# Performance work log

Measured on AMD Instinct MI355X. Metric: run time of the kernel, lower is better.

The kernel has to match this reference:

```python
import jax, jax.numpy as jnp
import numpy as np

N = 100_000      # nodes
E = 1_600_000    # edges
NG = 512         # graphs in batch
EPS = 1e-5


def _prop(x, src, dst, n, add_self_loops):
    """GCN-normalized sparse propagation: agg_i = sum_{j->i} d_j^-1/2 d_i^-1/2 x_j."""
    ones = jnp.ones(src.shape[0], x.dtype)
    deg = jax.ops.segment_sum(ones, dst, num_segments=n)
    if add_self_loops:
        deg = deg + 1.0
    dinv = jnp.where(deg > 0, jax.lax.rsqrt(jnp.maximum(deg, 1e-12)), 0.0)
    w = dinv[src] * dinv[dst]                       # [E]
    agg = jax.ops.segment_sum(x[src] * w[:, None], dst, num_segments=n)
    if add_self_loops:
        agg = agg + x * (dinv * dinv)[:, None]
    return agg


def setup_inputs() -> dict:
    key = jax.random.key(0)
    ks = jax.random.split(key, 24)
    w = lambda k, s: jax.random.normal(k, s, jnp.float32) * 0.05
    dim = 100
    return {
        "x": jax.random.normal(ks[0], (N, 128), jnp.float32),
        "src": jax.random.randint(ks[1], (E,), 0, N),
        "dst": jax.random.randint(ks[2], (E,), 0, N),
        "batch": jnp.sort(jax.random.randint(ks[3], (N,), 0, NG)),
        # SGConv 1 & 2 (propagate then Linear)
        "W1": w(ks[4], (128, dim)), "b1": jnp.zeros((dim,), jnp.float32),
        "W2": w(ks[5], (dim, dim)), "b2": jnp.zeros((dim,), jnp.float32),
        # BatchNorm1d affine params
        "gamma": jnp.ones((dim,), jnp.float32), "beta": jnp.zeros((dim,), jnp.float32),
        # ARMAConv (num_stacks=1, num_layers=1)
        "Wa_init": w(ks[6], (dim, dim)), "Wa_root": w(ks[7], (dim, dim)),
        "ba": jnp.zeros((dim,), jnp.float32),
        # MLP head
        "Wf1": w(ks[8], (dim, 2 * dim)), "bf1": jnp.zeros((2 * dim,), jnp.float32),
        "Wf2": w(ks[9], (2 * dim, 3 * dim)), "bf2": jnp.zeros((3 * dim,), jnp.float32),
        "Wf3": w(ks[10], (3 * dim, 2 * dim)), "bf3": jnp.zeros((2 * dim,), jnp.float32),
        "Wf4": w(ks[11], (2 * dim, 1)), "bf4": jnp.zeros((1,), jnp.float32),
    }


def reference(x, src, dst, batch, W1, b1, W2, b2, gamma, beta,
              Wa_init, Wa_root, ba, Wf1, bf1, Wf2, bf2, Wf3, bf3, Wf4, bf4):
    n = x.shape[0]
    # SGConv (K=1): propagate with self-loop gcn_norm, then linear; ReLU
    h = jax.nn.relu(_prop(x, src, dst, n, True) @ W1 + b1)
    h = jax.nn.relu(_prop(h, src, dst, n, True) @ W2 + b2)
    # BatchNorm1d (training mode: batch statistics, biased var)
    mu = jnp.mean(h, axis=0)
    var = jnp.mean((h - mu) ** 2, axis=0)
    h = (h - mu) * jax.lax.rsqrt(var + EPS) * gamma + beta
    # ARMAConv (1 stack, 1 layer): ReLU(A_hat (h W_init) + h W_root + b), no self-loops
    a = jax.nn.relu(_prop(h @ Wa_init, src, dst, n, False) + h @ Wa_root + ba)
    # global_add_pool over graph ids
    g = jax.ops.segment_sum(a, batch, num_segments=NG)   # [NG, dim]
    # MLP head
    g = jax.nn.relu(g @ Wf1 + bf1)
    g = jax.nn.relu(g @ Wf2 + bf2)
    g = jax.nn.relu(g @ Wf3 + bf3)
    return g @ Wf4 + bf4
```

## Files before the change

kernel.cpp:

```cpp
#include <hip/hip_runtime.h>
#include <hip/hip_fp16.h>

#define NNODES 100000
#define NEDGES 1600000
#define NGRAPH 512
#define DIM    100
#define DP     128
#define EPSBN  1e-5f
#define NBUK   ((NNODES + 255) >> 8)
#define BINCH  8192

typedef _Float16 half8 __attribute__((ext_vector_type(8)));
typedef float floatx4 __attribute__((ext_vector_type(4)));

__global__ __launch_bounds__(256) void bin_count_kernel(const int* __restrict__ dst,
                                                        int* __restrict__ btotal, int e) {
    __shared__ int lc[NBUK];
    int tid = threadIdx.x;
    int base = blockIdx.x * BINCH;
    int m = e - base; if (m > BINCH) m = BINCH;
    for (int b = tid; b < NBUK; b += 256) lc[b] = 0;
    __syncthreads();
    for (int j = tid; j < m; j += 256)
        atomicAdd(&lc[dst[base + j] >> 8], 1);
    __syncthreads();
    for (int b = tid; b < NBUK; b += 256)
        if (lc[b]) atomicAdd(&btotal[b], lc[b]);
}

__global__ void bucket_scan_kernel(const int* __restrict__ btotal, int* __restrict__ bbase,
                                   int* __restrict__ bcursor, int e) {
    __shared__ int s[512];
    int tid = threadIdx.x;
    int v = (tid < NBUK) ? btotal[tid] : 0;
    s[tid] = v; __syncthreads();
    for (int o = 1; o < 512; o <<= 1) {
        int t = (tid >= o) ? s[tid - o] : 0;
        __syncthreads();
        s[tid] += t;
        __syncthreads();
    }
    if (tid < NBUK) {
        int base = s[tid] - v;
        bbase[tid] = base;
        bcursor[tid] = base;
    }
    if (tid == 0) bbase[NBUK] = e;
}

__global__ __launch_bounds__(256) void bin_kernel(
        const int* __restrict__ src, const int* __restrict__ dst,
        int* __restrict__ bcursor, int2* __restrict__ gpairs, int e) {
    __shared__ int2 lpairs[BINCH];
    __shared__ int lcount[NBUK], lstart[NBUK], lcur[NBUK], gbase[NBUK];
    int tid = threadIdx.x;
    int base = blockIdx.x * BINCH;
    int m = e - base; if (m > BINCH) m = BINCH;

    for (int b = tid; b < NBUK; b += 256) lcount[b] = 0;
    __syncthreads();

    for (int j = tid; j < m; j += 256)
        atomicAdd(&lcount[dst[base + j] >> 8], 1);
    __syncthreads();

    if (tid == 0) {
        int acc = 0;
        for (int b = 0; b < NBUK; b++) {
            lstart[b] = acc;
            lcur[b] = acc;
            acc += lcount[b];
        }
    }
    __syncthreads();

    for (int b = tid; b < NBUK; b += 256)
        gbase[b] = atomicAdd(&bcursor[b], lcount[b]);
    for (int j = tid; j < m; j += 256) {
        int s = src[base + j], d = dst[base + j];
        int p = atomicAdd(&lcur[d >> 8], 1);
        lpairs[p] = make_int2(s, d);
    }
    __syncthreads();

    for (int j = tid; j < m; j += 256) {
        int2 pr = lpairs[j];
        int b = pr.y >> 8;
        gpairs[gbase[b] + (j - lstart[b])] = pr;
    }
}

__global__ __launch_bounds__(256) void bucket_build_kernel(
        const int2* __restrict__ gpairs, const int* __restrict__ bbase,
        int* __restrict__ off, int* __restrict__ ssorted,
        float* __restrict__ dsl, float* __restrict__ dnsl, int n, int e) {
    __shared__ int cnt[256];
    __shared__ int sc[256];
    int b = blockIdx.x, tid = threadIdx.x;
    int node0 = b << 8;
    int e0 = bbase[b], e1 = bbase[b + 1];

    cnt[tid] = 0;
    __syncthreads();
    for (int j = e0 + tid; j < e1; j += 256)
        atomicAdd(&cnt[gpairs[j].y & 255], 1);
    __syncthreads();

    int c = cnt[tid];
    sc[tid] = c; __syncthreads();
    for (int o = 1; o < 256; o <<= 1) {
        int t = (tid >= o) ? sc[tid - o] : 0;
        __syncthreads();
        sc[tid] += t;
        __syncthreads();
    }
    int excl = sc[tid] - c;

    int node = node0 + tid;
    if (node < n) {
        off[node] = e0 + excl;
        float cf = (float)c;
        dsl[node] = rsqrtf(cf + 1.0f);
        dnsl[node] = (c > 0) ? rsqrtf(cf) : 0.0f;
    }
    if (b == NBUK - 1 && tid == 0) off[n] = e;

    __syncthreads();
    cnt[tid] = e0 + excl;
    __syncthreads();
    for (int j = e0 + tid; j < e1; j += 256) {
        int2 pr = gpairs[j];
        int p = atomicAdd(&cnt[pr.y & 255], 1);
        ssorted[p] = pr.x;
    }
}

__global__ void prescale_kernel(const float* __restrict__ x, const float* __restrict__ d,
                                __half* __restrict__ yh, int n) {
    long i = (long)blockIdx.x * blockDim.x + threadIdx.x;
    if (i >= (long)n * 32) return;
    int row = (int)(i >> 5);
    float s = d[row];
    float4 v = ((const float4*)x)[i];
    __half2 p01 = __floats2half2_rn(v.x * s, v.y * s);
    __half2 p23 = __floats2half2_rn(v.z * s, v.w * s);
    uint2 u;
    u.x = *(unsigned int*)&p01;
    u.y = *(unsigned int*)&p23;
    ((uint2*)yh)[i] = u;
}

__global__ void packW_kernel(const float* __restrict__ W, _Float16* __restrict__ WtF,
                             int K, int Kout) {
    int idx = blockIdx.x * 256 + threadIdx.x;
    if (idx >= DP * DP) return;
    int j = idx & 7;
    int l = (idx >> 3) & 63;
    int c = idx >> 9;
    int t = c >> 2, k0 = c & 3;
    int nn = t * 16 + (l & 15);
    int k = k0 * 32 + (l >> 4) * 8 + j;
    float v = (k < K && nn < Kout) ? W[k * Kout + nn] : 0.f;
    WtF[idx] = (_Float16)v;
}

__global__ __launch_bounds__(256) void prop_kernel(
        const __half* __restrict__ pre, const int* __restrict__ ssorted,
        const int* __restrict__ off, const float* __restrict__ dinv,
        __half* __restrict__ outH, int n, int selfloop) {
    int wave = (blockIdx.x * blockDim.x + threadIdx.x) >> 6;
    int lane = threadIdx.x & 63;
    if (wave >= n) return;
    int e0 = off[wave], e1 = off[wave + 1];
    int deg = e1 - e0;
    int g = lane >> 4;
    int q = lane & 15;

    float acc[8];
#pragma unroll
    for (int i = 0; i < 8; i++) acc[i] = 0.f;

    auto addu = [&](uint4 u) {
        float2 f;
        f = __half22float2(*(__half2*)&u.x); acc[0] += f.x; acc[1] += f.y;
        f = __half22float2(*(__half2*)&u.y); acc[2] += f.x; acc[3] += f.y;
        f = __half22float2(*(__half2*)&u.z); acc[4] += f.x; acc[5] += f.y;
        f = __half22float2(*(__half2*)&u.w); acc[6] += f.x; acc[7] += f.y;
    };
    auto rowptr = [&](int s) -> const uint4* {
        return (const uint4*)&pre[(long)s * DP + q * 8];
    };

    for (int base = 0; base < deg; base += 64) {
        int m = deg - base; if (m > 64) m = 64;
        int sidx = (lane < m) ? ssorted[e0 + base + lane] : 0;
        int j = 0;
        for (; j + 16 <= m; j += 16) {
            int s0 = __shfl(sidx, j + g);
            int s1 = __shfl(sidx, j + 4 + g);
            int s2 = __shfl(sidx, j + 8 + g);
            int s3 = __shfl(sidx, j + 12 + g);
            uint4 u0 = *rowptr(s0);
            uint4 u1 = *rowptr(s1);
            uint4 u2 = *rowptr(s2);
            uint4 u3 = *rowptr(s3);
            addu(u0); addu(u1); addu(u2); addu(u3);
        }
        for (; j + 4 <= m; j += 4) {
            int s = __shfl(sidx, j + g);
            addu(*rowptr(s));
        }
        if (j < m) {
            int r = m - j;
            int s = __shfl(sidx, (g < r) ? j + g : j);
            if (g < r) addu(*rowptr(s));
        }
    }

#pragma unroll
    for (int i = 0; i < 8; i++) {
        acc[i] += __shfl_xor(acc[i], 16);
        acc[i] += __shfl_xor(acc[i], 32);
    }

    if (g == 0) {
        float dn = dinv[wave];
        if (selfloop) addu(*rowptr(wave));
        __half2 p0 = __floats2half2_rn(dn * acc[0], dn * acc[1]);
        __half2 p1 = __floats2half2_rn(dn * acc[2], dn * acc[3]);
        __half2 p2 = __floats2half2_rn(dn * acc[4], dn * acc[5]);
        __half2 p3 = __floats2half2_rn(dn * acc[6], dn * acc[7]);
        uint4 u;
        u.x = *(unsigned int*)&p0;
        u.y = *(unsigned int*)&p1;
        u.z = *(unsigned int*)&p2;
        u.w = *(unsigned int*)&p3;
        *(uint4*)&outH[(long)wave * DP + q * 8] = u;
    }
}

__global__ __launch_bounds__(256) void prop_arma_kernel(
        const __half* __restrict__ pre, const int* __restrict__ ssorted,
        const int* __restrict__ off, const float* __restrict__ dinv,
        const __half* __restrict__ R, __half* __restrict__ outH, int n) {
    int wave = (blockIdx.x * blockDim.x + threadIdx.x) >> 6;
    int lane = threadIdx.x & 63;
    if (wave >= n) return;
    int e0 = off[wave], e1 = off[wave + 1];
    int deg = e1 - e0;
    int g = lane >> 4;
    int q = lane & 15;

    float acc[8];
#pragma unroll
    for (int i = 0; i < 8; i++) acc[i] = 0.f;

    auto addu = [&](uint4 u) {
        float2 f;
        f = __half22float2(*(__half2*)&u.x); acc[0] += f.x; acc[1] += f.y;
        f = __half22float2(*(__half2*)&u.y); acc[2] += f.x; acc[3] += f.y;
        f = __half22float2(*(__half2*)&u.z); acc[4] += f.x; acc[5] += f.y;
        f = __half22float2(*(__half2*)&u.w); acc[6] += f.x; acc[7] += f.y;
    };
    auto rowptr = [&](int s) -> const uint4* {
        return (const uint4*)&pre[(long)s * DP + q * 8];
    };

    for (int base = 0; base < deg; base += 64) {
        int m = deg - base; if (m > 64) m = 64;
        int sidx = (lane < m) ? ssorted[e0 + base + lane] : 0;
        int j = 0;
        for (; j + 16 <= m; j += 16) {
            int s0 = __shfl(sidx, j + g);
            int s1 = __shfl(sidx, j + 4 + g);
            int s2 = __shfl(sidx, j + 8 + g);
            int s3 = __shfl(sidx, j + 12 + g);
            uint4 u0 = *rowptr(s0);
            uint4 u1 = *rowptr(s1);
            uint4 u2 = *rowptr(s2);
            uint4 u3 = *rowptr(s3);
            addu(u0); addu(u1); addu(u2); addu(u3);
        }
        for (; j + 4 <= m; j += 4) {
            int s = __shfl(sidx, j + g);
            addu(*rowptr(s));
        }
        if (j < m) {
            int r = m - j;
            int s = __shfl(sidx, (g < r) ? j + g : j);
            if (g < r) addu(*rowptr(s));
        }
    }

#pragma unroll
    for (int i = 0; i < 8; i++) {
        acc[i] += __shfl_xor(acc[i], 16);
        acc[i] += __shfl_xor(acc[i], 32);
    }

    if (g == 0) {
        float dn = dinv[wave];
        uint4 r4 = *(const uint4*)&R[(long)wave * DP + q * 8];
        float rr[8];
        float2 f;
        f = __half22float2(*(__half2*)&r4.x); rr[0] = f.x; rr[1] = f.y;
        f = __half22float2(*(__half2*)&r4.y); rr[2] = f.x; rr[3] = f.y;
        f = __half22float2(*(__half2*)&r4.z); rr[4] = f.x; rr[5] = f.y;
        f = __half22float2(*(__half2*)&r4.w); rr[6] = f.x; rr[7] = f.y;
        float o[8];
#pragma unroll
        for (int i = 0; i < 8; i++) o[i] = fmaxf(dn * acc[i] + rr[i], 0.f);
        __half2 p0 = __floats2half2_rn(o[0], o[1]);
        __half2 p1 = __floats2half2_rn(o[2], o[3]);
        __half2 p2 = __floats2half2_rn(o[4], o[5]);
        __half2 p3 = __floats2half2_rn(o[6], o[7]);
        uint4 u;
        u.x = *(unsigned int*)&p0;
        u.y = *(unsigned int*)&p1;
        u.z = *(unsigned int*)&p2;
        u.w = *(unsigned int*)&p3;
        *(uint4*)&outH[(long)wave * DP + q * 8] = u;
    }
}

__global__ __launch_bounds__(256, 2) void matmul_mfma_kernel(
        const __half* __restrict__ A, const _Float16* __restrict__ WtF,
        const float* __restrict__ bias, const float* __restrict__ rowscale,
        __half* __restrict__ Ch, float* __restrict__ bnsum, float* __restrict__ bnsq,
        int M, int Kout, int relu) {
    __shared__ float Ct[64 * 132];
    int tid = threadIdx.x;
    int wave = tid >> 6;
    int lane = tid & 63;
    int m16 = lane & 15;
    int quad = lane >> 4;
    long row0blk = (long)blockIdx.x * 64;
    long row0 = row0blk + wave * 16;

    const half8* Bp = (const half8*)WtF;
    half8 bf[32];
#pragma unroll
    for (int c = 0; c < 32; c++) bf[c] = Bp[c * 64 + lane];

    half8 af[4];
    {
        long ar = row0 + m16; if (ar >= M) ar = M - 1;
        const _Float16* Ap = (const _Float16*)&A[ar * DP + quad * 8];
#pragma unroll
        for (int k0 = 0; k0 < 4; k0++)
            af[k0] = *(const half8*)(Ap + k0 * 32);
    }

    floatx4 acc[8];
#pragma unroll
    for (int t = 0; t < 8; t++) acc[t] = (floatx4){0.f, 0.f, 0.f, 0.f};

#pragma unroll
    for (int c = 0; c < 32; c++)
        acc[c >> 2] = __builtin_amdgcn_mfma_f32_16x16x32_f16(af[c & 3], bf[c], acc[c >> 2], 0, 0, 0);

    int lrow0 = wave * 16 + quad * 4;
#pragma unroll
    for (int t = 0; t < 8; t++)
#pragma unroll
        for (int r = 0; r < 4; r++)
            Ct[(lrow0 + r) * 132 + t * 16 + m16] = acc[t][r];
    __syncthreads();

    float s4[4] = {0.f, 0.f, 0.f, 0.f};
    float q4[4] = {0.f, 0.f, 0.f, 0.f};
    for (int idx = tid; idx < 64 * 32; idx += 256) {
        int lr = idx >> 5, c4 = idx & 31;
        long grow = row0blk + lr;
        if (grow >= M) continue;
        int col = c4 * 4;
        float4 v = *(const float4*)&Ct[lr * 132 + col];
        if (bias && col < Kout) {
            float4 bb = *(const float4*)&bias[col];
            v.x += bb.x; v.y += bb.y; v.z += bb.z; v.w += bb.w;
        }
        if (relu) {
            v.x = fmaxf(v.x, 0.f); v.y = fmaxf(v.y, 0.f);
            v.z = fmaxf(v.z, 0.f); v.w = fmaxf(v.w, 0.f);
        }
        if (rowscale) {
            float rs = rowscale[grow];
            v.x *= rs; v.y *= rs; v.z *= rs; v.w *= rs;
        }
        if (bnsum) {
            s4[0] += v.x; s4[1] += v.y; s4[2] += v.z; s4[3] += v.w;
            q4[0] += v.x * v.x; q4[1] += v.y * v.y; q4[2] += v.z * v.z; q4[3] += v.w * v.w;
        }
        __half2 p01 = __floats2half2_rn(v.x, v.y);
        __half2 p23 = __floats2half2_rn(v.z, v.w);
        uint2 u;
        u.x = *(unsigned int*)&p01;
        u.y = *(unsigned int*)&p23;
        *(uint2*)&Ch[grow * DP + col] = u;
    }

    if (bnsum) {
        __syncthreads();
        float* scr = Ct;
        int g = tid >> 5, c4 = tid & 31;
#pragma unroll
        for (int i = 0; i < 4; i++) {
            scr[g * 128 + c4 * 4 + i] = s4[i];
            scr[1024 + g * 128 + c4 * 4 + i] = q4[i];
        }
        __syncthreads();
        if (tid < 128) {
            float ss = 0.f, qq = 0.f;
#pragma unroll
            for (int gg = 0; gg < 8; gg++) {
                ss += scr[gg * 128 + tid];
                qq += scr[1024 + gg * 128 + tid];
            }
            atomicAdd(&bnsum[tid], ss);
            atomicAdd(&bnsq[tid], qq);
        }
    }
}

__global__ __launch_bounds__(256, 2) void matmul_dual_kernel(
        const __half* __restrict__ A, const _Float16* __restrict__ WtF3,
        const _Float16* __restrict__ WtF4, const float* __restrict__ ba,
        const float* __restrict__ rowscale,
        __half* __restrict__ Ch1, __half* __restrict__ ChR, int M, int Kout) {
    __shared__ float Ct[64 * 132];
    int tid = threadIdx.x;
    int wave = tid >> 6;
    int lane = tid & 63;
    int m16 = lane & 15;
    int quad = lane >> 4;
    long row0blk = (long)blockIdx.x * 64;
    long row0 = row0blk + wave * 16;

    half8 af[4];
    {
        long ar = row0 + m16; if (ar >= M) ar = M - 1;
        const _Float16* Ap = (const _Float16*)&A[ar * DP + quad * 8];
#pragma unroll
        for (int k0 = 0; k0 < 4; k0++)
            af[k0] = *(const half8*)(Ap + k0 * 32);
    }

    const half8* Bp3 = (const half8*)WtF3;
    const half8* Bp4 = (const half8*)WtF4;
    floatx4 acc3[8], acc4[8];
#pragma unroll
    for (int t = 0; t < 8; t++) {
        acc3[t] = (floatx4){0.f, 0.f, 0.f, 0.f};
        acc4[t] = (floatx4){0.f, 0.f, 0.f, 0.f};
    }

#pragma unroll
    for (int t = 0; t < 8; t++) {
        half8 b3[4], b4[4];
#pragma unroll
        for (int k0 = 0; k0 < 4; k0++) {
            b3[k0] = Bp3[(t * 4 + k0) * 64 + lane];
            b4[k0] = Bp4[(t * 4 + k0) * 64 + lane];
        }
#pragma unroll
        for (int k0 = 0; k0 < 4; k0++) {
            acc3[t] = __builtin_amdgcn_mfma_f32_16x16x32_f16(af[k0], b3[k0], acc3[t], 0, 0, 0);
            acc4[t] = __builtin_amdgcn_mfma_f32_16x16x32_f16(af[k0], b4[k0], acc4[t], 0, 0, 0);
        }
    }

    int lrow0 = wave * 16 + quad * 4;

#pragma unroll
    for (int t = 0; t < 8; t++)
#pragma unroll
        for (int r = 0; r < 4; r++)
            Ct[(lrow0 + r) * 132 + t * 16 + m16] = acc3[t][r];
    __syncthreads();
    for (int idx = tid; idx < 64 * 32; idx += 256) {
        int lr = idx >> 5, c4 = idx & 31;
        long grow = row0blk + lr;
        if (grow >= M) continue;
        int col = c4 * 4;
        float4 v = *(const float4*)&Ct[lr * 132 + col];
        float rs = rowscale[grow];
        v.x *= rs; v.y *= rs; v.z *= rs; v.w *= rs;
        __half2 p01 = __floats2half2_rn(v.x, v.y);
        __half2 p23 = __floats2half2_rn(v.z, v.w);
        uint2 u;
        u.x = *(unsigned int*)&p01;
        u.y = *(unsigned int*)&p23;
        *(uint2*)&Ch1[grow * DP + col] = u;
    }
    __syncthreads();

#pragma unroll
    for (int t = 0; t < 8; t++)
#pragma unroll
        for (int r = 0; r < 4; r++)
            Ct[(lrow0 + r) * 132 + t * 16 + m16] = acc4[t][r];
    __syncthreads();
    for (int idx = tid; idx < 64 * 32; idx += 256) {
        int lr = idx >> 5, c4 = idx & 31;
        long grow = row0blk + lr;
        if (grow >= M) continue;
        int col = c4 * 4;
        float4 v = *(const float4*)&Ct[lr * 132 + col];
        if (col < Kout) {
            float4 bb = *(const float4*)&ba[col];
            v.x += bb.x; v.y += bb.y; v.z += bb.z; v.w += bb.w;
        }
        __half2 p01 = __floats2half2_rn(v.x, v.y);
        __half2 p23 = __floats2half2_rn(v.z, v.w);
        uint2 u;
        u.x = *(unsigned int*)&p01;
        u.y = *(unsigned int*)&p23;
        *(uint2*)&ChR[grow * DP + col] = u;
    }
}

__global__ void bn_prep_kernel(const float* __restrict__ sum, const float* __restrict__ sq,
                               const float* __restrict__ gamma, const float* __restrict__ beta,
                               float* __restrict__ scale, float* __restrict__ shift, int n) {
    int c = threadIdx.x;
    float sc = 0.f, sh = 0.f;
    if (c < DIM) {
        float inv_n = 1.0f / (float)n;
        float mu = sum[c] * inv_n;
        float var = sq[c] * inv_n - mu * mu;
        float rs = rsqrtf(var + EPSBN);
        sc = rs * gamma[c];
        sh = beta[c] - mu * sc;
    }
    scale[c] = sc;
    shift[c] = sh;
}

__global__ void bn_apply_kernel(__half* __restrict__ h, const float* __restrict__ scale,
                                const float* __restrict__ shift, int n) {
    long i = (long)blockIdx.x * blockDim.x + threadIdx.x;
    if (i >= (long)n * 16) return;
    int cb = (int)(i & 15) * 8;
    uint4 u = ((const uint4*)h)[i];
    __half2* hp = (__half2*)&u;
    uint4 o;
    __half2* op = (__half2*)&o;
#pragma unroll
    for (int p = 0; p < 4; p++) {
        float2 f = __half22float2(hp[p]);
        int c = cb + p * 2;
        f.x = f.x * scale[c] + shift[c];
        f.y = f.y * scale[c + 1] + shift[c + 1];
        op[p] = __floats2half2_rn(f.x, f.y);
    }
    ((uint4*)h)[i] = o;
}

__global__ void gbounds_kernel(const int* __restrict__ batch, int* __restrict__ gstart, int n) {
    int g = threadIdx.x;
    int lo = 0, hi = n;
    while (lo < hi) {
        int mid = (lo + hi) >> 1;
        if (batch[mid] < g) lo = mid + 1; else hi = mid;
    }
    gstart[g] = lo;
    if (g == 0) gstart[NGRAPH] = n;
}

__global__ __launch_bounds__(512) void pool_kernel(const __half* __restrict__ a,
                                                   const int* __restrict__ gstart,
                                                   float* __restrict__ g) {
    __shared__ float2 red[512];
    int b = blockIdx.x, tid = threadIdx.x;
    int col2 = tid & 63;
    int rgrp = tid >> 6;
    int lo = gstart[b], hi = gstart[b + 1];
    float2 s = make_float2(0.f, 0.f);
    for (int r = lo + rgrp; r < hi; r += 8) {
        __half2 h = *(const __half2*)&a[(long)r * DP + col2 * 2];
        float2 f = __half22float2(h);
        s.x += f.x; s.y += f.y;
    }
    red[tid] = s;
    __syncthreads();
    if (tid < 64) {
        float2 t = make_float2(0.f, 0.f);
#pragma unroll
        for (int gg = 0; gg < 8; gg++) {
            float2 v = red[gg * 64 + tid];
            t.x += v.x; t.y += v.y;
        }
        *(float2*)&g[b * DP + tid * 2] = t;
    }
}

__global__ __launch_bounds__(256) void mlp_kernel(
        const float* __restrict__ g,
        const float* __restrict__ Wf1, const float* __restrict__ bf1,
        const float* __restrict__ Wf2, const float* __restrict__ bf2,
        const float* __restrict__ Wf3, const float* __restrict__ bf3,
        const float* __restrict__ Wf4, const float* __restrict__ bf4,
        float* __restrict__ out) {
    __shared__ float a0[100], a1[200], a2[300], a3[200], red[256];
    int b = blockIdx.x, tid = threadIdx.x;
    if (tid < 100) a0[tid] = g[b * DP + tid];
    __syncthreads();
    for (int c = tid; c < 200; c += 256) {
        float s = bf1[c];
        for (int k = 0; k < 100; k++) s += a0[k] * Wf1[k * 200 + c];
        a1[c] = fmaxf(s, 0.f);
    }
    __syncthreads();
    for (int c = tid; c < 300; c += 256) {
        float s = bf2[c];
        for (int k = 0; k < 200; k++) s += a1[k] * Wf2[k * 300 + c];
        a2[c] = fmaxf(s, 0.f);
    }
    __syncthreads();
    for (int c = tid; c < 200; c += 256) {
        float s = bf3[c];
        for (int k = 0; k < 300; k++) s += a2[k] * Wf3[k * 200 + c];
        a3[c] = fmaxf(s, 0.f);
    }
    __syncthreads();
    red[tid] = (tid < 200) ? a3[tid] * Wf4[tid] : 0.f;
    __syncthreads();
    for (int o = 128; o > 0; o >>= 1) {
        if (tid < o) red[tid] += red[tid + o];
        __syncthreads();
    }
    if (tid == 0) out[b] = red[0] + bf4[0];
}

extern "C" void kernel_launch(void* const* d_in, const int* in_sizes, int n_in,
                              void* d_out, int out_size, void* d_ws, size_t ws_size,
                              hipStream_t stream) {
    const float* x      = (const float*)d_in[0];
    const int*   src    = (const int*)d_in[1];
    const int*   dst    = (const int*)d_in[2];
    const int*   batch  = (const int*)d_in[3];
    const float* W1     = (const float*)d_in[4];
    const float* b1     = (const float*)d_in[5];
    const float* W2     = (const float*)d_in[6];
    const float* b2     = (const float*)d_in[7];
    const float* gamma  = (const float*)d_in[8];
    const float* beta   = (const float*)d_in[9];
    const float* Wa_init= (const float*)d_in[10];
    const float* Wa_root= (const float*)d_in[11];
    const float* ba     = (const float*)d_in[12];
    const float* Wf1    = (const float*)d_in[13];
    const float* bf1    = (const float*)d_in[14];
    const float* Wf2    = (const float*)d_in[15];
    const float* bf2    = (const float*)d_in[16];
    const float* Wf3    = (const float*)d_in[17];
    const float* bf3    = (const float*)d_in[18];
    const float* Wf4    = (const float*)d_in[19];
    const float* bf4    = (const float*)d_in[20];
    float* out = (float*)d_out;

    const int n = NNODES;
    const int e = NEDGES;

    char* ws = (char*)d_ws;
    auto carve = [&](size_t bytes) -> void* {
        void* p = (void*)ws;
        ws += (bytes + 255) & ~(size_t)255;
        return p;
    };
    __half* bufH    = (__half*)carve((size_t)n * DP * 2);
    __half* bufHA   = (__half*)carve((size_t)n * DP * 2);
    __half* bufHB   = (__half*)carve((size_t)n * DP * 2);
    __half* bufR    = (__half*)carve((size_t)n * DP * 2);
    __half* bufHC   = (__half*)carve((size_t)n * DP * 2);
    _Float16* Wt1   = (_Float16*)carve((size_t)DP * DP * 2);
    _Float16* Wt2   = (_Float16*)carve((size_t)DP * DP * 2);
    _Float16* Wt3   = (_Float16*)carve((size_t)DP * DP * 2);
    _Float16* Wt4   = (_Float16*)carve((size_t)DP * DP * 2);
    int*    off     = (int*)carve((size_t)(n + 1) * 4);
    int*    btotal  = (int*)carve((size_t)NBUK * 4);
    int*    bbase   = (int*)carve((size_t)(NBUK + 1) * 4);
    int*    bcursor = (int*)carve((size_t)NBUK * 4);
    int*    ssorted = (int*)carve((size_t)e * 4);
    int2*   gpairs  = (int2*)carve((size_t)e * 8);
    float*  dinv_sl = (float*)carve((size_t)n * 4);
    float*  dinv_nsl= (float*)carve((size_t)n * 4);
    float*  bnsum   = (float*)carve(DP * 4);
    float*  bnsq    = (float*)carve(DP * 4);
    float*  bnscale = (float*)carve(DP * 4);
    float*  bnshift = (float*)carve(DP * 4);
    int*    gstart  = (int*)carve((size_t)(NGRAPH + 1) * 4);
    float*  gpool   = (float*)carve((size_t)NGRAPH * DP * 4);

    const int wblk = (DP * DP + 255) / 256;
    const int nchunk = (e + BINCH - 1) / BINCH;

    packW_kernel<<<wblk, 256, 0, stream>>>(W1, Wt1, 128, DIM);
    packW_kernel<<<wblk, 256, 0, stream>>>(W2, Wt2, DIM, DIM);
    packW_kernel<<<wblk, 256, 0, stream>>>(Wa_init, Wt3, DIM, DIM);
    packW_kernel<<<wblk, 256, 0, stream>>>(Wa_root, Wt4, DIM, DIM);

    hipMemsetAsync(btotal, 0, (size_t)NBUK * 4, stream);
    hipMemsetAsync(bnsum, 0, DP * 4, stream);
    hipMemsetAsync(bnsq, 0, DP * 4, stream);
    bin_count_kernel<<<nchunk, 256, 0, stream>>>(dst, btotal, e);
    bucket_scan_kernel<<<1, 512, 0, stream>>>(btotal, bbase, bcursor, e);
    bin_kernel<<<nchunk, 256, 0, stream>>>(src, dst, bcursor, gpairs, e);
    bucket_build_kernel<<<NBUK, 256, 0, stream>>>(gpairs, bbase, off, ssorted, dinv_sl, dinv_nsl, n, e);
    gbounds_kernel<<<1, 512, 0, stream>>>(batch, gstart, n);

    const int prop_blocks = (n + 3) / 4;
    const int mm_blocks = (n + 63) / 64;

    prescale_kernel<<<(int)(((long)n * 32 + 255) / 256), 256, 0, stream>>>(x, dinv_sl, bufH, n);
    prop_kernel<<<prop_blocks, 256, 0, stream>>>(bufH, ssorted, off, dinv_sl, bufHA, n, 1);
    matmul_mfma_kernel<<<mm_blocks, 256, 0, stream>>>(bufHA, Wt1, b1, dinv_sl, bufH, nullptr, nullptr, n, DIM, 1);

    prop_kernel<<<prop_blocks, 256, 0, stream>>>(bufH, ssorted, off, dinv_sl, bufHA, n, 1);
    matmul_mfma_kernel<<<mm_blocks, 256, 0, stream>>>(bufHA, Wt2, b2, nullptr, bufHB, bnsum, bnsq, n, DIM, 1);

    bn_prep_kernel<<<1, 128, 0, stream>>>(bnsum, bnsq, gamma, beta, bnscale, bnshift, n);
    bn_apply_kernel<<<(int)(((long)n * 16 + 255) / 256), 256, 0, stream>>>(bufHB, bnscale, bnshift, n);

    matmul_dual_kernel<<<mm_blocks, 256, 0, stream>>>(bufHB, Wt3, Wt4, ba, dinv_nsl, bufH, bufR, n, DIM);
    prop_arma_kernel<<<prop_blocks, 256, 0, stream>>>(bufH, ssorted, off, dinv_nsl, bufR, bufHC, n);

    pool_kernel<<<NGRAPH, 512, 0, stream>>>(bufHC, gstart, gpool);

    mlp_kernel<<<NGRAPH, 256, 0, stream>>>(gpool, Wf1, bf1, Wf2, bf2, Wf3, bf3, Wf4, bf4, out);
}
```

Measured before the change: 564.1 us.

## Fuse BatchNorm apply into dual matmul, stage weights in LDS, merge packW launches

Drops the separate bn_apply pass and instead applies the BatchNorm scale and shift to the A fragments as they are loaded in the dual matmul, removing one full read-write pass over the hidden activations. Both matmul kernels now stage the packed fp16 weights in shared memory, reusing the Ct buffer, rather than holding 32 half8 fragments in registers. The launch_bounds occupancy hint is dropped, and the four packW launches are merged into one. This trades register pressure for extra LDS traffic and barriers, and the per-element BN math adds work to the matmul.

```diff
diff --git a/kernel.cpp b/kernel.cpp
--- a/kernel.cpp
+++ b/kernel.cpp
@@ -59,11 +59,9 @@
 
     for (int b = tid; b < NBUK; b += 256) lcount[b] = 0;
     __syncthreads();
-
     for (int j = tid; j < m; j += 256)
         atomicAdd(&lcount[dst[base + j] >> 8], 1);
     __syncthreads();
-
     if (tid == 0) {
         int acc = 0;
         for (int b = 0; b < NBUK; b++) {
@@ -73,7 +71,6 @@
         }
     }
     __syncthreads();
-
     for (int b = tid; b < NBUK; b += 256)
         gbase[b] = atomicAdd(&bcursor[b], lcount[b]);
     for (int j = tid; j < m; j += 256) {
@@ -82,7 +79,6 @@
         lpairs[p] = make_int2(s, d);
     }
     __syncthreads();
-
     for (int j = tid; j < m; j += 256) {
         int2 pr = lpairs[j];
         int b = pr.y >> 8;
@@ -150,18 +146,24 @@
     ((uint2*)yh)[i] = u;
 }
 
-__global__ void packW_kernel(const float* __restrict__ W, _Float16* __restrict__ WtF,
-                             int K, int Kout) {
-    int idx = blockIdx.x * 256 + threadIdx.x;
-    if (idx >= DP * DP) return;
+__global__ void packW4_kernel(const float* __restrict__ W1, const float* __restrict__ W2,
+                              const float* __restrict__ W3, const float* __restrict__ W4,
+                              _Float16* __restrict__ Wt1, _Float16* __restrict__ Wt2,
+                              _Float16* __restrict__ Wt3, _Float16* __restrict__ Wt4) {
+    int which = blockIdx.x >> 6;
+    int idx = (blockIdx.x & 63) * 256 + threadIdx.x;
+    const float* W = (which == 0) ? W1 : (which == 1) ? W2 : (which == 2) ? W3 : W4;
+    _Float16* Wt  = (which == 0) ? Wt1 : (which == 1) ? Wt2 : (which == 2) ? Wt3 : Wt4;
+    int K = (which == 0) ? 128 : DIM;
     int j = idx & 7;
     int l = (idx >> 3) & 63;
     int c = idx >> 9;
     int t = c >> 2, k0 = c & 3;
     int nn = t * 16 + (l & 15);
     int k = k0 * 32 + (l >> 4) * 8 + j;
-    float v = (k < K && nn < Kout) ? W[k * Kout + nn] : 0.f;
-    WtF[idx] = (_Float16)v;
+    float v = (k < K && nn < DIM) ? W[k * DIM + nn] : 0.f;
+    if (which == 0) v = (k < 128 && nn < DIM) ? W[k * DIM + nn] : 0.f;
+    Wt[idx] = (_Float16)v;
 }
 
 __global__ __launch_bounds__(256) void prop_kernel(
@@ -323,12 +325,14 @@
     }
 }
 
-__global__ __launch_bounds__(256, 2) void matmul_mfma_kernel(
+__global__ __launch_bounds__(256) void matmul_mfma_kernel(
         const __half* __restrict__ A, const _Float16* __restrict__ WtF,
         const float* __restrict__ bias, const float* __restrict__ rowscale,
         __half* __restrict__ Ch, float* __restrict__ bnsum, float* __restrict__ bnsq,
         int M, int Kout, int relu) {
-    __shared__ float Ct[64 * 132];
+    __shared__ char smraw[64 * 132 * 4];
+    _Float16* Bs = (_Float16*)smraw;
+    float* Ct = (float*)smraw;
     int tid = threadIdx.x;
     int wave = tid >> 6;
     int lane = tid & 63;
@@ -337,10 +341,11 @@
     long row0blk = (long)blockIdx.x * 64;
     long row0 = row0blk + wave * 16;
 
-    const half8* Bp = (const half8*)WtF;
-    half8 bf[32];
-#pragma unroll
-    for (int c = 0; c < 32; c++) bf[c] = Bp[c * 64 + lane];
+    {
+        const uint4* s = (const uint4*)WtF;
+        uint4* d = (uint4*)Bs;
+        for (int i = tid; i < 2048; i += 256) d[i] = s[i];
+    }
 
     half8 af[4];
     {
@@ -350,14 +355,18 @@
         for (int k0 = 0; k0 < 4; k0++)
             af[k0] = *(const half8*)(Ap + k0 * 32);
     }
+    __syncthreads();
 
     floatx4 acc[8];
 #pragma unroll
     for (int t = 0; t < 8; t++) acc[t] = (floatx4){0.f, 0.f, 0.f, 0.f};
 
 #pragma unroll
-    for (int c = 0; c < 32; c++)
-        acc[c >> 2] = __builtin_amdgcn_mfma_f32_16x16x32_f16(af[c & 3], bf[c], acc[c >> 2], 0, 0, 0);
+    for (int c = 0; c < 32; c++) {
+        half8 bf = *(const half8*)&Bs[(c * 64 + lane) * 8];
+        acc[c >> 2] = __builtin_amdgcn_mfma_f32_16x16x32_f16(af[c & 3], bf, acc[c >> 2], 0, 0, 0);
+    }
+    __syncthreads();
 
     int lrow0 = wave * 16 + quad * 4;
 #pragma unroll
@@ -422,12 +431,15 @@
     }
 }
 
-__global__ __launch_bounds__(256, 2) void matmul_dual_kernel(
+__global__ __launch_bounds__(256) void matmul_dual_kernel(
         const __half* __restrict__ A, const _Float16* __restrict__ WtF3,
         const _Float16* __restrict__ WtF4, const float* __restrict__ ba,
         const float* __restrict__ rowscale,
+        const float* __restrict__ bnscale, const float* __restrict__ bnshift,
         __half* __restrict__ Ch1, __half* __restrict__ ChR, int M, int Kout) {
-    __shared__ float Ct[64 * 132];
+    __shared__ char smraw[64 * 132 * 4];
+    _Float16* Bs = (_Float16*)smraw;
+    float* Ct = (float*)smraw;
     int tid = threadIdx.x;
     int wave = tid >> 6;
     int lane = tid & 63;
@@ -441,12 +453,26 @@
         long ar = row0 + m16; if (ar >= M) ar = M - 1;
         const _Float16* Ap = (const _Float16*)&A[ar * DP + quad * 8];
 #pragma unroll
-        for (int k0 = 0; k0 < 4; k0++)
-            af[k0] = *(const half8*)(Ap + k0 * 32);
-    }
-
-    const half8* Bp3 = (const half8*)WtF3;
-    const half8* Bp4 = (const half8*)WtF4;
+        for (int k0 = 0; k0 < 4; k0++) {
+            half8 h = *(const half8*)(Ap + k0 * 32);
+            int c0 = quad * 8 + k0 * 32;
+            float4 sc0 = *(const float4*)&bnscale[c0];
+            float4 sc1 = *(const float4*)&bnscale[c0 + 4];
+            float4 sh0 = *(const float4*)&bnshift[c0];
+            float4 sh1 = *(const float4*)&bnshift[c0 + 4];
+            half8 o;
+            o[0] = (_Float16)((float)h[0] * sc0.x + sh0.x);
+            o[1] = (_Float16)((float)h[1] * sc0.y + sh0.y);
+            o[2] = (_Float16)((float)h[2] * sc0.z + sh0.z);
+            o[3] = (_Float16)((float)h[3] * sc0.w + sh0.w);
+            o[4] = (_Float16)((float)h[4] * sc1.x + sh1.x);
+            o[5] = (_Float16)((float)h[5] * sc1.y + sh1.y);
+            o[6] = (_Float16)((float)h[6] * sc1.z + sh1.z);
+            o[7] = (_Float16)((float)h[7] * sc1.w + sh1.w);
+            af[k0] = o;
+        }
+    }
+
     floatx4 acc3[8], acc4[8];
 #pragma unroll
     for (int t = 0; t < 8; t++) {
@@ -454,20 +480,31 @@
         acc4[t] = (floatx4){0.f, 0.f, 0.f, 0.f};
     }
 
-#pragma unroll
-    for (int t = 0; t < 8; t++) {
-        half8 b3[4], b4[4];
-#pragma unroll
-        for (int k0 = 0; k0 < 4; k0++) {
-            b3[k0] = Bp3[(t * 4 + k0) * 64 + lane];
-            b4[k0] = Bp4[(t * 4 + k0) * 64 + lane];
-        }
-#pragma unroll
-        for (int k0 = 0; k0 < 4; k0++) {
-            acc3[t] = __builtin_amdgcn_mfma_f32_16x16x32_f16(af[k0], b3[k0], acc3[t], 0, 0, 0);
-            acc4[t] = __builtin_amdgcn_mfma_f32_16x16x32_f16(af[k0], b4[k0], acc4[t], 0, 0, 0);
-        }
-    }
+    {
+        const uint4* s = (const uint4*)WtF3;
+        uint4* d = (uint4*)Bs;
+        for (int i = tid; i < 2048; i += 256) d[i] = s[i];
+    }
+    __syncthreads();
+#pragma unroll
+    for (int c = 0; c < 32; c++) {
+        half8 bf = *(const half8*)&Bs[(c * 64 + lane) * 8];
+        acc3[c >> 2] = __builtin_amdgcn_mfma_f32_16x16x32_f16(af[c & 3], bf, acc3[c >> 2], 0, 0, 0);
+    }
+    __syncthreads();
+
+    {
+        const uint4* s = (const uint4*)WtF4;
+        uint4* d = (uint4*)Bs;
+        for (int i = tid; i < 2048; i += 256) d[i] = s[i];
+    }
+    __syncthreads();
+#pragma unroll
+    for (int c = 0; c < 32; c++) {
+        half8 bf = *(const half8*)&Bs[(c * 64 + lane) * 8];
+        acc4[c >> 2] = __builtin_amdgcn_mfma_f32_16x16x32_f16(af[c & 3], bf, acc4[c >> 2], 0, 0, 0);
+    }
+    __syncthreads();
 
     int lrow0 = wave * 16 + quad * 4;
 
@@ -534,26 +571,6 @@
     }
     scale[c] = sc;
     shift[c] = sh;
-}
-
-__global__ void bn_apply_kernel(__half* __restrict__ h, const float* __restrict__ scale,
-                                const float* __restrict__ shift, int n) {
-    long i = (long)blockIdx.x * blockDim.x + threadIdx.x;
-    if (i >= (long)n * 16) return;
-    int cb = (int)(i & 15) * 8;
-    uint4 u = ((const uint4*)h)[i];
-    __half2* hp = (__half2*)&u;
-    uint4 o;
-    __half2* op = (__half2*)&o;
-#pragma unroll
-    for (int p = 0; p < 4; p++) {
-        float2 f = __half22float2(hp[p]);
-        int c = cb + p * 2;
-        f.x = f.x * scale[c] + shift[c];
-        f.y = f.y * scale[c + 1] + shift[c + 1];
-        op[p] = __floats2half2_rn(f.x, f.y);
-    }
-    ((uint4*)h)[i] = o;
 }
 
 __global__ void gbounds_kernel(const int* __restrict__ batch, int* __restrict__ gstart, int n) {
@@ -691,13 +708,9 @@
     int*    gstart  = (int*)carve((size_t)(NGRAPH + 1) * 4);
     float*  gpool   = (float*)carve((size_t)NGRAPH * DP * 4);
 
-    const int wblk = (DP * DP + 255) / 256;
     const int nchunk = (e + BINCH - 1) / BINCH;
 
-    packW_kernel<<<wblk, 256, 0, stream>>>(W1, Wt1, 128, DIM);
-    packW_kernel<<<wblk, 256, 0, stream>>>(W2, Wt2, DIM, DIM);
-    packW_kernel<<<wblk, 256, 0, stream>>>(Wa_init, Wt3, DIM, DIM);
-    packW_kernel<<<wblk, 256, 0, stream>>>(Wa_root, Wt4, DIM, DIM);
+    packW4_kernel<<<256, 256, 0, stream>>>(W1, W2, Wa_init, Wa_root, Wt1, Wt2, Wt3, Wt4);
 
     hipMemsetAsync(btotal, 0, (size_t)NBUK * 4, stream);
     hipMemsetAsync(bnsum, 0, DP * 4, stream);
@@ -719,9 +732,8 @@
     matmul_mfma_kernel<<<mm_blocks, 256, 0, stream>>>(bufHA, Wt2, b2, nullptr, bufHB, bnsum, bnsq, n, DIM, 1);
 
     bn_prep_kernel<<<1, 128, 0, stream>>>(bnsum, bnsq, gamma, beta, bnscale, bnshift, n);
-    bn_apply_kernel<<<(int)(((long)n * 16 + 255) / 256), 256, 0, stream>>>(bufHB, bnscale, bnshift, n);
-
-    matmul_dual_kernel<<<mm_blocks, 256, 0, stream>>>(bufHB, Wt3, Wt4, ba, dinv_nsl, bufH, bufR, n, DIM);
+
+    matmul_dual_kernel<<<mm_blocks, 256, 0, stream>>>(bufHB, Wt3, Wt4, ba, dinv_nsl, bnscale, bnshift, bufH, bufR, n, DIM);
     prop_arma_kernel<<<prop_blocks, 256, 0, stream>>>(bufH, ssorted, off, dinv_nsl, bufR, bufHC, n);
 
     pool_kernel<<<NGRAPH, 512, 0, stream>>>(bufHC, gstart, gpool);
```

Result: faster. 545.9 us (-3.2%).
